# Optimization experiments

Measured on AMD Instinct MI355X. Metric: run time of the kernel, lower is better.

## Reference

```python
import jax, jax.numpy as jnp
import numpy as np

B, T, H, A, E, V = 32, 128, 1024, 1024, 512, 512  # A==H required by the module's cat/Linear shapes


def setup_inputs() -> dict:
    key = jax.random.key(0)
    ks = jax.random.split(key, 13)
    s = 0.02
    return {
        "encoder_outputs": jax.random.normal(ks[0], (B, A, E), jnp.float32),
        "hidden": jax.random.normal(ks[1], (1, B, H), jnp.float32),
        "target_seq": jax.random.normal(ks[2], (B, T, H), jnp.float32),
        "W_att": jax.random.normal(ks[3], (H + A, A), jnp.float32) * s,
        "b_att": jax.random.normal(ks[4], (A,), jnp.float32) * s,
        "W_comb": jax.random.normal(ks[5], (H + E, H), jnp.float32) * s,
        "b_comb": jax.random.normal(ks[6], (H,), jnp.float32) * s,
        "W_ih": jax.random.normal(ks[7], (3 * H, H), jnp.float32) * s,
        "b_ih": jax.random.normal(ks[8], (3 * H,), jnp.float32) * s,
        "W_hh": jax.random.normal(ks[9], (3 * H, H), jnp.float32) * s,
        "b_hh": jax.random.normal(ks[10], (3 * H,), jnp.float32) * s,
        "W_out": jax.random.normal(ks[11], (H, V), jnp.float32) * s,
        "b_out": jax.random.normal(ks[12], (V,), jnp.float32) * s,
    }


def reference(encoder_outputs, hidden, target_seq, W_att, b_att, W_comb, b_comb,
              W_ih, b_ih, W_hh, b_hh, W_out, b_out):
    # Teacher forcing: decoder input at step t is zeros (t=0) then target_seq[:, t-1]
    dec_in = jnp.concatenate([jnp.zeros_like(target_seq[:, :1]), target_seq[:, :-1]], axis=1)  # [B,T,H]
    dec_ts = jnp.swapaxes(dec_in, 0, 1)  # [T,B,H]

    def step(h, dec):  # h: [B,H], dec: [B,H]
        # attention over encoder positions (softmax width A == encoder seq len)
        attn = jax.nn.softmax(jnp.concatenate([dec, h], axis=1) @ W_att + b_att, axis=1)  # [B,A]
        ctx = jnp.einsum('bl,ble->be', attn, encoder_outputs)  # [B,E]
        g = jax.nn.relu(jnp.concatenate([dec, ctx], axis=1) @ W_comb + b_comb)  # [B,H]
        # GRU cell (torch gate order r, z, n)
        gi = g @ W_ih.T + b_ih
        gh = h @ W_hh.T + b_hh
        ir, iz, i_n = jnp.split(gi, 3, axis=1)
        hr, hz, h_n = jnp.split(gh, 3, axis=1)
        r = jax.nn.sigmoid(ir + hr)
        z = jax.nn.sigmoid(iz + hz)
        n = jnp.tanh(i_n + r * h_n)
        h_new = (1.0 - z) * n + z * h
        out_tok = h_new @ W_out + b_out  # [B,V]
        return h_new, out_tok

    h_last, outs = jax.lax.scan(step, hidden[0], dec_ts)  # outs: [T,B,V]
    output_seq = jnp.swapaxes(outs, 0, 1)  # [B,T,V]
    return output_seq, h_last[None]
```

## Files before the change

kernel.cpp:

```cpp
#include <hip/hip_runtime.h>

typedef unsigned short u16;
typedef unsigned int u32;
typedef unsigned long long u64;
typedef short v8s __attribute__((ext_vector_type(8)));
typedef float v4f __attribute__((ext_vector_type(4)));
typedef int v4i __attribute__((ext_vector_type(4)));

#define MFMA16(a, b, c) __builtin_amdgcn_mfma_f32_16x16x32_bf16((a), (b), (c), 0, 0, 0)

#define B_ 32
#define T_ 128
#define H_ 1024
#define A_ 1024
#define E_ 512
#define V_ 512
#define NBLK 256
#define NTH 512
#define NSLOT 32
#define ENC_LDS_BYTES 131072
#define SCRATCH_BYTES 28672
#define DSMEM_BYTES (ENC_LDS_BYTES + SCRATCH_BYTES)

__device__ __forceinline__ float b2f(u16 u) {
  union { u32 u; float f; } c; c.u = ((u32)u) << 16; return c.f;
}
__device__ __forceinline__ u16 f2b(float f) {
  union { float f; u32 u; } c; c.f = f;
  u32 x = c.u;
  x += 0x7fffu + ((x >> 16) & 1u);
  return (u16)(x >> 16);
}

__device__ __forceinline__ void ato_st(u32* p, u32 v) {
  __hip_atomic_store(p, v, __ATOMIC_RELAXED, __HIP_MEMORY_SCOPE_AGENT);
}
__device__ __forceinline__ void ato_stf(float* p, float v) {
  union { float f; u32 u; } c; c.f = v; ato_st((u32*)p, c.u);
}
__device__ __forceinline__ void ato_addf(float* p, float v) {
  __hip_atomic_fetch_add(p, v, __ATOMIC_RELAXED, __HIP_MEMORY_SCOPE_AGENT);
}

__device__ __forceinline__ v4i ld16_sc1(const void* p) {
  v4i r;
  asm volatile("global_load_dwordx4 %0, %1, off sc1" : "=v"(r) : "v"(p));
  return r;
}
__device__ __forceinline__ float ld4_sc1(const void* p) {
  float r;
  asm volatile("global_load_dword %0, %1, off sc1" : "=v"(r) : "v"(p));
  return r;
}
__device__ __forceinline__ void wait_vm0() {
  asm volatile("s_waitcnt vmcnt(0)" ::: "memory");
  __builtin_amdgcn_sched_barrier(0);
}
__device__ __forceinline__ v8s as8(v4i x) { union { v4i a; v8s b; } u; u.a = x; return u.b; }
__device__ __forceinline__ void cvt8(v4i qa, v4i qb, v8s& hi, v8s& lo) {
  union { v4i q; float f[4]; } a, b;
  a.q = qa; b.q = qb;
  float v[8] = {a.f[0], a.f[1], a.f[2], a.f[3], b.f[0], b.f[1], b.f[2], b.f[3]};
  u16 hh[8], ll[8];
  #pragma unroll
  for (int i = 0; i < 8; ++i) {
    float x = fmaxf(v[i], 0.f);
    u16 hv = f2b(x);
    hh[i] = hv; ll[i] = f2b(x - b2f(hv));
  }
  hi = *(v8s*)hh; lo = *(v8s*)ll;
}

__device__ __forceinline__ void grid_bar(u32* arr, u32 ep) {
  asm volatile("s_waitcnt vmcnt(0)" ::: "memory");
  __syncthreads();
  if (threadIdx.x == 0)
    __hip_atomic_store(arr + blockIdx.x * NSLOT, ep, __ATOMIC_RELAXED, __HIP_MEMORY_SCOPE_AGENT);
  if (threadIdx.x < NBLK) {
    while (__hip_atomic_load(arr + threadIdx.x * NSLOT, __ATOMIC_RELAXED, __HIP_MEMORY_SCOPE_AGENT) < ep)
      __builtin_amdgcn_s_sleep(1);
  }
  __syncthreads();
  asm volatile("" ::: "memory");
}

__device__ __forceinline__ void gemm_nk(const u16* ah, const u16* al, size_t mstr,
                                        const u16* bp, int nk, v4f& c0, v4f& c1) {
  #pragma unroll 2
  for (int i = 0; i < nk; ++i) {
    v8s b   = *(const v8s*)(bp);
    v8s a0h = *(const v8s*)(ah);
    v8s a1h = *(const v8s*)(ah + mstr);
    v8s a0l = *(const v8s*)(al);
    v8s a1l = *(const v8s*)(al + mstr);
    c0 = MFMA16(a0h, b, c0);
    c1 = MFMA16(a1h, b, c1);
    c0 = MFMA16(a0l, b, c0);
    c1 = MFMA16(a1l, b, c1);
    ah += 32; al += 32; bp += 32;
  }
}

__device__ __forceinline__ void red_store2(float* part, int wv, int lane, v4f c0, v4f c1) {
  float* p = part + (wv * 64 + lane) * 8;
  #pragma unroll
  for (int r = 0; r < 4; ++r) { p[r] = c0[r]; p[4 + r] = c1[r]; }
}
__device__ __forceinline__ float red_sum2(const float* part, int o) {
  int m = o >> 4, n = o & 15;
  int lane = (((m & 15) >> 2) << 4) + n;
  int idx = ((m >> 4) << 2) + (m & 3);
  float s = 0.f;
  #pragma unroll
  for (int w = 0; w < 8; ++w) s += part[(w * 64 + lane) * 8 + idx];
  return s;
}

__global__ void __launch_bounds__(NTH, 1)
dec_persist(const u16* __restrict__ tgt_hi, const u16* __restrict__ tgt_lo,
            const u16* __restrict__ WattT, const u16* __restrict__ Whh_b,
            const u16* __restrict__ Wih_b, const u16* __restrict__ WcombT,
            const u16* __restrict__ Wc_ctx,
            const float* __restrict__ enc_f,
            const float* __restrict__ batt, const float* __restrict__ bcomb,
            const float* __restrict__ bih, const float* __restrict__ bhh,
            float* h, float* logit, float* gh, float* g_acc, float* logit_dec,
            u16* hbf_hi, u16* hbf_lo, u16* hseqb, u32* bar)
{
  const int tid = threadIdx.x;
  const int bid = blockIdx.x;
  const int lane = tid & 63;
  const int wv = tid >> 6;
  const int ln = lane & 15;
  const int kq8 = (lane >> 4) * 8;

  extern __shared__ __align__(16) unsigned char dsm[];
  u16* lds_enc = (u16*)dsm;
  float* scratch = (float*)(dsm + ENC_LDS_BYTES);

  {
    int b = bid >> 3, e0 = (bid & 7) * 64;
    const float* src = enc_f + (size_t)b * A_ * E_ + e0 + (tid & 7) * 8;
    int seg = (tid & 7) * 8;
    for (int i = 0; i < 16; ++i) {
      int row = i * 64 + (tid >> 3);
      const float* sp = src + (size_t)row * E_;
      float4 a = *(const float4*)sp;
      float4 bq = *(const float4*)(sp + 4);
      u16 tmp[8] = {f2b(a.x), f2b(a.y), f2b(a.z), f2b(a.w),
                    f2b(bq.x), f2b(bq.y), f2b(bq.z), f2b(bq.w)};
      *(v8s*)(lds_enc + row * 64 + seg) = *(v8s*)tmp;
    }
  }

  u32 ep = 0;

  for (int t = 0; t < T_; ++t) {
    {
      float* part = scratch;
      size_t a0 = (size_t)ln * H_ + wv * 128 + kq8;
      v4i ah0[4], ah1[4], al0[4], al1[4];
      #pragma unroll
      for (int i = 0; i < 4; ++i) {
        ah0[i] = ld16_sc1(hbf_hi + a0 + i * 32);
        ah1[i] = ld16_sc1(hbf_hi + a0 + 16 * H_ + i * 32);
        al0[i] = ld16_sc1(hbf_lo + a0 + i * 32);
        al1[i] = ld16_sc1(hbf_lo + a0 + 16 * H_ + i * 32);
      }
      float ldec = 0.f;
      const u16* bp;
      int n0;
      if (bid < 64) {
        int gi = bid * 512 + tid;
        ato_stf(&g_acc[((t + 1) & 1) * (B_ * H_) + gi], bcomb[gi & (H_ - 1)]);
        n0 = bid * 16;
        ldec = ld4_sc1(&logit_dec[(t & 1) * (B_ * A_) + (tid >> 4) * A_ + n0 + (tid & 15)]);
        bp = WattT + (size_t)(n0 + ln) * 2048 + 1024 + wv * 128 + kq8;
      } else {
        n0 = (bid - 64) * 16;
        bp = Whh_b + (size_t)(n0 + ln) * H_ + wv * 128 + kq8;
      }
      v8s wb[4];
      #pragma unroll
      for (int i = 0; i < 4; ++i) wb[i] = *(const v8s*)(bp + i * 32);
      v4f c0 = {0.f, 0.f, 0.f, 0.f}, c1 = {0.f, 0.f, 0.f, 0.f};
      wait_vm0();
      #pragma unroll
      for (int i = 0; i < 4; ++i) {
        c0 = MFMA16(as8(ah0[i]), wb[i], c0);
        c1 = MFMA16(as8(ah1[i]), wb[i], c1);
        c0 = MFMA16(as8(al0[i]), wb[i], c0);
        c1 = MFMA16(as8(al1[i]), wb[i], c1);
      }
      red_store2(part, wv, lane, c0, c1);
      __syncthreads();
      {
        float s = red_sum2(part, tid);
        int m = tid >> 4, n = tid & 15;
        if (bid < 64) {
          ato_stf(&logit[m * A_ + n0 + n], s + ldec + batt[n0 + n]);
        } else {
          ato_stf(&gh[(size_t)(n0 + n) * 32 + m], s + bhh[n0 + n]);
        }
      }
    }
    grid_bar(bar, ++ep);

    {
      float* p    = scratch;
      float* part = scratch + 1024;
      float* red  = scratch + 5120;
      float* sctx = scratch + 5136;
      int b = bid >> 3, es = bid & 7;
      float v1 = ld4_sc1(&logit[b * A_ + tid]);
      float v2 = ld4_sc1(&logit[b * A_ + 512 + tid]);
      wait_vm0();
      float mx = fmaxf(v1, v2);
      #pragma unroll
      for (int off = 32; off; off >>= 1) mx = fmaxf(mx, __shfl_xor(mx, off));
      if (lane == 0) red[wv] = mx;
      __syncthreads();
      float mfull = red[0];
      #pragma unroll
      for (int q = 1; q < 8; ++q) mfull = fmaxf(mfull, red[q]);
      float e1 = __expf(v1 - mfull), e2 = __expf(v2 - mfull);
      p[tid] = e1; p[512 + tid] = e2;
      float sm = e1 + e2;
      #pragma unroll
      for (int off = 32; off; off >>= 1) sm += __shfl_xor(sm, off);
      if (lane == 0) red[8 + wv] = sm;
      __syncthreads();
      float ssum = red[8];
      #pragma unroll
      for (int q = 1; q < 8; ++q) ssum += red[8 + q];
      float inv = 1.f / ssum;

      int le = lane & 7, lr = lane >> 3;
      float acc[8] = {0.f, 0.f, 0.f, 0.f, 0.f, 0.f, 0.f, 0.f};
      #pragma unroll 4
      for (int i = 0; i < 16; ++i) {
        int l = i * 64 + wv * 8 + lr;
        v8s w = *(const v8s*)(lds_enc + l * 64 + le * 8);
        float pv = p[l];
        #pragma unroll
        for (int r = 0; r < 8; ++r) acc[r] += pv * b2f((u16)w[r]);
      }
      float* pp = part + ((wv * 8 + lr) * 8 + le) * 8;
      #pragma unroll
      for (int r = 0; r < 8; ++r) pp[r] = acc[r];
      __syncthreads();
      if (tid < 64) {
        int eo = tid >> 3, r = tid & 7;
        float s = 0.f;
        #pragma unroll
        for (int q = 0; q < 64; ++q) s += part[q * 64 + eo * 8 + r];
        sctx[tid] = s * inv;
      }
      __syncthreads();
      {
        const u16* wrow = Wc_ctx + (size_t)(es * 64) * H_ + tid * 2;
        float a0 = 0.f, a1 = 0.f;
        #pragma unroll 4
        for (int e = 0; e < 64; ++e) {
          u32 w = *(const u32*)(wrow + (size_t)e * H_);
          float pv = sctx[e];
          a0 += pv * b2f((u16)w);
          a1 += pv * b2f((u16)(w >> 16));
        }
        float* gp = g_acc + (t & 1) * (B_ * H_) + b * H_ + tid * 2;
        ato_addf(gp, a0);
        ato_addf(gp + 1, a1);
      }
    }
    grid_bar(bar, ++ep);

    {
      if (bid < 64) {
        float* part = scratch;
        float* hx   = scratch + 6144;
        int j0 = bid * 16;
        const float* gbase = g_acc + (t & 1) * (B_ * H_);
        int koff0 = wv * 128 + kq8;
        v4i gr0[8], gr1[8];
        #pragma unroll
        for (int i = 0; i < 4; ++i) {
          const float* p0 = gbase + (size_t)ln * H_ + koff0 + i * 32;
          const float* p1 = gbase + (size_t)(ln + 16) * H_ + koff0 + i * 32;
          gr0[2 * i]     = ld16_sc1(p0);
          gr0[2 * i + 1] = ld16_sc1(p0 + 4);
          gr1[2 * i]     = ld16_sc1(p1);
          gr1[2 * i + 1] = ld16_sc1(p1 + 4);
        }
        const u16* bp0 = Wih_b + (size_t)(j0 + ln) * H_ + koff0;
        const u16* bp1 = bp0 + (size_t)H_ * H_;
        const u16* bp2 = bp0 + (size_t)2 * H_ * H_;
        v8s wb0[4], wb1[4], wb2[4];
        #pragma unroll
        for (int i = 0; i < 4; ++i) {
          wb0[i] = *(const v8s*)(bp0 + i * 32);
          wb1[i] = *(const v8s*)(bp1 + i * 32);
          wb2[i] = *(const v8s*)(bp2 + i * 32);
        }
        v4f c00 = {0.f,0.f,0.f,0.f}, c01 = c00, c02 = c00, c10 = c00, c11 = c00, c12 = c00;
        wait_vm0();
        #pragma unroll
        for (int i = 0; i < 4; ++i) {
          v8s a0h, a0l, a1h, a1l;
          cvt8(gr0[2 * i], gr0[2 * i + 1], a0h, a0l);
          cvt8(gr1[2 * i], gr1[2 * i + 1], a1h, a1l);
          c00 = MFMA16(a0h, wb0[i], c00); c00 = MFMA16(a0l, wb0[i], c00);
          c01 = MFMA16(a0h, wb1[i], c01); c01 = MFMA16(a0l, wb1[i], c01);
          c02 = MFMA16(a0h, wb2[i], c02); c02 = MFMA16(a0l, wb2[i], c02);
          c10 = MFMA16(a1h, wb0[i], c10); c10 = MFMA16(a1l, wb0[i], c10);
          c11 = MFMA16(a1h, wb1[i], c11); c11 = MFMA16(a1l, wb1[i], c11);
          c12 = MFMA16(a1h, wb2[i], c12); c12 = MFMA16(a1l, wb2[i], c12);
        }
        float hr0 = 0.f, hz0 = 0.f, hn0 = 0.f, hr1 = 0.f, hz1 = 0.f, hn1 = 0.f;
        float ho0 = 0.f, ho1 = 0.f;
        int obl = tid >> 4, jj = tid & 15, j = j0 + jj;
        if (tid < 256) {
          hr0 = ld4_sc1(&gh[(size_t)j * 32 + obl]);
          hz0 = ld4_sc1(&gh[(size_t)(H_ + j) * 32 + obl]);
          hn0 = ld4_sc1(&gh[(size_t)(2 * H_ + j) * 32 + obl]);
          hr1 = ld4_sc1(&gh[(size_t)j * 32 + 16 + obl]);
          hz1 = ld4_sc1(&gh[(size_t)(H_ + j) * 32 + 16 + obl]);
          hn1 = ld4_sc1(&gh[(size_t)(2 * H_ + j) * 32 + 16 + obl]);
          ho0 = h[obl * H_ + j];
          ho1 = h[(obl + 16) * H_ + j];
        }
        float bi_r = 0.f, bi_z = 0.f, bi_n = 0.f;
        if (tid < 256) {
          bi_r = bih[j]; bi_z = bih[H_ + j]; bi_n = bih[2 * H_ + j];
        }
        #pragma unroll
        for (int pass = 0; pass < 2; ++pass) {
          float* pp = part + (wv * 64 + lane) * 12;
          if (pass == 0) {
            #pragma unroll
            for (int r = 0; r < 4; ++r) { pp[r] = c00[r]; pp[4 + r] = c01[r]; pp[8 + r] = c02[r]; }
          } else {
            #pragma unroll
            for (int r = 0; r < 4; ++r) { pp[r] = c10[r]; pp[4 + r] = c11[r]; pp[8 + r] = c12[r]; }
          }
          __syncthreads();
          if (tid < 256) {
            if (pass == 0) wait_vm0();
            int ob = pass * 16 + obl;
            int lanei = ((obl >> 2) << 4) + jj;
            int rg = obl & 3;
            float ir = 0.f, iz = 0.f, in_ = 0.f;
            #pragma unroll
            for (int w = 0; w < 8; ++w) {
              const float* q = part + (w * 64 + lanei) * 12;
              ir += q[rg]; iz += q[4 + rg]; in_ += q[8 + rg];
            }
            ir += bi_r; iz += bi_z; in_ += bi_n;
            float hr = pass ? hr1 : hr0;
            float hz = pass ? hz1 : hz0;
            float hn = pass ? hn1 : hn0;
            float ho = pass ? ho1 : ho0;
            float r = 1.f / (1.f + __expf(-(ir + hr)));
            float z = 1.f / (1.f + __expf(-(iz + hz)));
            float n = tanhf(in_ + r * hn);
            float hnew = (1.f - z) * n + z * ho;
            h[ob * H_ + j] = hnew;
            hx[ob * 16 + jj] = hnew;
          }
          __syncthreads();
        }
        if (tid < 256) {
          int ob2 = tid >> 3, j2 = (tid & 7) * 2;
          float v0 = hx[ob2 * 16 + j2], v1 = hx[ob2 * 16 + j2 + 1];
          u16 h0 = f2b(v0), h1 = f2b(v1);
          u16 l0 = f2b(v0 - b2f(h0)), l1 = f2b(v1 - b2f(h1));
          int idx = ob2 * H_ + j0 + j2;
          u32 hp = (u32)h0 | ((u32)h1 << 16);
          ato_st((u32*)(hbf_hi + idx), hp);
          ato_st((u32*)(hbf_lo + idx), (u32)l0 | ((u32)l1 << 16));
          *(u32*)(hseqb + ((size_t)t * 32 + ob2) * H_ + j0 + j2) = hp;
        }
      } else if (bid < 128) {
        if (t < T_ - 1) {
          float* part = scratch;
          int n0 = (bid - 64) * 16;
          v4f c0 = {0.f, 0.f, 0.f, 0.f}, c1 = {0.f, 0.f, 0.f, 0.f};
          size_t abase = ((size_t)ln * T_ + t) * H_ + wv * 128 + kq8;
          const u16* bp = WattT + (size_t)(n0 + ln) * 2048 + wv * 128 + kq8;
          gemm_nk(tgt_hi + abase, tgt_lo + abase, (size_t)16 * T_ * H_, bp, 4, c0, c1);
          red_store2(part, wv, lane, c0, c1);
          __syncthreads();
          int m = tid >> 4, n = tid & 15;
          ato_stf(&logit_dec[((t + 1) & 1) * (B_ * A_) + m * A_ + n0 + n], red_sum2(part, tid));
        }
      } else if (bid < 192) {
        if (t < T_ - 1) {
          float* part = scratch;
          int n0 = (bid - 128) * 16;
          v4f c0 = {0.f, 0.f, 0.f, 0.f}, c1 = {0.f, 0.f, 0.f, 0.f};
          size_t abase = ((size_t)ln * T_ + t) * H_ + wv * 128 + kq8;
          const u16* bp = WcombT + (size_t)(n0 + ln) * 1536 + wv * 128 + kq8;
          gemm_nk(tgt_hi + abase, tgt_lo + abase, (size_t)16 * T_ * H_, bp, 4, c0, c1);
          red_store2(part, wv, lane, c0, c1);
          __syncthreads();
          int m = tid >> 4, n = tid & 15;
          ato_addf(&g_acc[((t + 1) & 1) * (B_ * H_) + m * H_ + n0 + n], red_sum2(part, tid));
        }
      }
    }
    grid_bar(bar, ++ep);
  }
}

__global__ void __launch_bounds__(256, 2)
out_gemm(const u16* __restrict__ hseqb, const u16* __restrict__ WoutT,
         const float* __restrict__ bout, float* __restrict__ out)
{
  int tid = threadIdx.x, lane = tid & 63, wv = tid >> 6;
  int ln = lane & 15, kq8 = (lane >> 4) * 8;
  int m0 = (blockIdx.x >> 3) * 32;
  int n0 = (blockIdx.x & 7) * 64 + wv * 16;
  v4f c0 = {0.f, 0.f, 0.f, 0.f}, c1 = {0.f, 0.f, 0.f, 0.f};
  const u16* ap = hseqb + (size_t)(m0 + ln) * 1024 + kq8;
  const u16* bp = WoutT + (size_t)(n0 + ln) * 1024 + kq8;
  for (int i = 0; i < 32; ++i) {
    v8s b = *(const v8s*)bp;
    v8s a0 = *(const v8s*)ap;
    v8s a1 = *(const v8s*)(ap + 16 * 1024);
    c0 = MFMA16(a0, b, c0);
    c1 = MFMA16(a1, b, c1);
    ap += 32; bp += 32;
  }
  int v = n0 + ln;
  float bo = bout[v];
  int rbase = (lane >> 4) * 4;
  #pragma unroll
  for (int rg = 0; rg < 4; ++rg) {
    int m = m0 + rbase + rg;
    out[((size_t)(m & 31) * T_ + (m >> 5)) * V_ + v] = c0[rg] + bo;
    int m2 = m + 16;
    out[((size_t)(m2 & 31) * T_ + (m2 >> 5)) * V_ + v] = c1[rg] + bo;
  }
}

__global__ void __launch_bounds__(256)
hlast_copy(const float* __restrict__ h, float* __restrict__ out)
{
  int i = blockIdx.x * 256 + threadIdx.x;
  if (i < B_ * H_) out[(size_t)B_ * T_ * V_ + i] = h[i];
}

__global__ void __launch_bounds__(256)
k_cvt(const float* __restrict__ in, u16* __restrict__ out, int n)
{
  int stride = gridDim.x * 256;
  for (int i = blockIdx.x * 256 + threadIdx.x; i < n; i += stride) out[i] = f2b(in[i]);
}

__global__ void __launch_bounds__(256)
k_cvt_split(const float* __restrict__ in, u16* __restrict__ hi, u16* __restrict__ lo, int n)
{
  int stride = gridDim.x * 256;
  for (int i = blockIdx.x * 256 + threadIdx.x; i < n; i += stride) {
    float x = in[i];
    u16 a = f2b(x);
    hi[i] = a;
    lo[i] = f2b(x - b2f(a));
  }
}

__global__ void __launch_bounds__(256)
k_tr(const float* __restrict__ in, u16* __restrict__ out, int R, int C)
{
  __shared__ float tile[32][33];
  int tc = C >> 5;
  int r0 = (blockIdx.x / tc) << 5, c0 = (blockIdx.x % tc) << 5;
  int tx = threadIdx.x & 31, ty = threadIdx.x >> 5;
  #pragma unroll
  for (int q = 0; q < 4; ++q) {
    int r = ty + q * 8;
    tile[r][tx] = in[(size_t)(r0 + r) * C + c0 + tx];
  }
  __syncthreads();
  #pragma unroll
  for (int q = 0; q < 4; ++q) {
    int r = ty + q * 8;
    out[(size_t)(c0 + r) * R + r0 + tx] = f2b(tile[tx][r]);
  }
}

__global__ void __launch_bounds__(256)
k_init(const float* __restrict__ hidden, const float* __restrict__ bcomb,
       float* h, u16* hhi, u16* hlo, float* g_acc)
{
  int i = blockIdx.x * 256 + threadIdx.x;
  if (i < B_ * H_) {
    float x = hidden[i];
    h[i] = x;
    u16 a = f2b(x);
    hhi[i] = a;
    hlo[i] = f2b(x - b2f(a));
    g_acc[i] = bcomb[i & (H_ - 1)];
  }
}

extern "C" void kernel_launch(void* const* d_in, const int* in_sizes, int n_in,
                              void* d_out, int out_size, void* d_ws, size_t ws_size,
                              hipStream_t stream) {
  (void)in_sizes; (void)n_in; (void)out_size; (void)ws_size;
  const float* enc    = (const float*)d_in[0];
  const float* hidden = (const float*)d_in[1];
  const float* tgt    = (const float*)d_in[2];
  const float* Watt   = (const float*)d_in[3];
  const float* batt   = (const float*)d_in[4];
  const float* Wcomb  = (const float*)d_in[5];
  const float* bcomb  = (const float*)d_in[6];
  const float* Wih    = (const float*)d_in[7];
  const float* bih    = (const float*)d_in[8];
  const float* Whh    = (const float*)d_in[9];
  const float* bhh    = (const float*)d_in[10];
  const float* Wout   = (const float*)d_in[11];
  const float* bout   = (const float*)d_in[12];

  size_t off = 0;
  char* base = (char*)d_ws;
  auto alloc = [&](size_t bytes) -> void* {
    void* p = base + off;
    off += (bytes + 255) & ~(size_t)255;
    return p;
  };
  size_t bar_bytes = (size_t)(NBLK * NSLOT + NSLOT) * 4;
  u32*   bar    = (u32*)  alloc(bar_bytes);
  float* h      = (float*)alloc(B_ * H_ * 4);
  float* logit  = (float*)alloc(B_ * A_ * 4);
  float* gh     = (float*)alloc((size_t)3 * H_ * B_ * 4);
  float* g_acc  = (float*)alloc((size_t)2 * B_ * H_ * 4);
  float* logit_dec = (float*)alloc((size_t)2 * B_ * A_ * 4);
  u16*   hbf_hi = (u16*)  alloc(B_ * H_ * 2);
  u16*   hbf_lo = (u16*)  alloc(B_ * H_ * 2);
  u16*   hseqb  = (u16*)  alloc((size_t)T_ * B_ * H_ * 2);
  u16*   tgt_hi = (u16*)  alloc((size_t)B_ * T_ * H_ * 2);
  u16*   tgt_lo = (u16*)  alloc((size_t)B_ * T_ * H_ * 2);
  u16*   WattT  = (u16*)  alloc((size_t)2048 * 1024 * 2);
  u16*   Whh_b  = (u16*)  alloc((size_t)3 * H_ * H_ * 2);
  u16*   Wih_b  = (u16*)  alloc((size_t)3 * H_ * H_ * 2);
  u16*   WcombT = (u16*)  alloc((size_t)1024 * 1536 * 2);
  u16*   Wc_ctx = (u16*)  alloc((size_t)512 * 1024 * 2);
  u16*   WoutT  = (u16*)  alloc((size_t)512 * 1024 * 2);

  hipMemsetAsync(bar, 0, bar_bytes, stream);
  hipMemsetAsync(logit_dec, 0, (size_t)2 * B_ * A_ * 4, stream);

  k_cvt_split<<<2048, 256, 0, stream>>>(tgt, tgt_hi, tgt_lo, B_ * T_ * H_);
  k_cvt<<<2048, 256, 0, stream>>>(Whh, Whh_b, 3 * H_ * H_);
  k_cvt<<<2048, 256, 0, stream>>>(Wih, Wih_b, 3 * H_ * H_);
  k_cvt<<<2048, 256, 0, stream>>>(Wcomb + (size_t)1024 * H_, Wc_ctx, 512 * H_);
  k_tr<<<64 * 32, 256, 0, stream>>>(Watt, WattT, 2048, 1024);
  k_tr<<<48 * 32, 256, 0, stream>>>(Wcomb, WcombT, 1536, 1024);
  k_tr<<<32 * 16, 256, 0, stream>>>(Wout, WoutT, 1024, 512);
  k_init<<<128, 256, 0, stream>>>(hidden, bcomb, h, hbf_hi, hbf_lo, g_acc);

  hipFuncSetAttribute((const void*)dec_persist,
                      hipFuncAttributeMaxDynamicSharedMemorySize, DSMEM_BYTES);

  dec_persist<<<NBLK, NTH, DSMEM_BYTES, stream>>>(tgt_hi, tgt_lo, WattT, Whh_b, Wih_b,
                                                  WcombT, Wc_ctx, enc,
                                                  batt, bcomb, bih, bhh,
                                                  h, logit, gh, g_acc, logit_dec,
                                                  hbf_hi, hbf_lo, hseqb, bar);
  out_gemm<<<1024, 256, 0, stream>>>(hseqb, WoutT, bout, (float*)d_out);
  hlast_copy<<<128, 256, 0, stream>>>(h, (float*)d_out);
}
```

Baseline: 3.641 ms.

## Hoist teacher-forced input GEMMs out of persistent loop; add two-level grid barrier

The decoder-input projections through W_att and W_comb no longer run inside the persistent recurrent kernel. They are now computed for all timesteps by a separate batched GEMM kernel into full-sequence buffers, with the biases folded in, so each step only reads a precomputed value. The grid barrier becomes two-level: 8 aggregator blocks each watch 32 block flags, and every block then polls only 8 flags. The context-weight matrix is transposed so each thread reads it with vector loads. The cost is larger workspace buffers and two extra kernel launches, in exchange for less per-step work and less barrier polling.

```diff
diff --git a/kernel.cpp b/kernel.cpp
--- a/kernel.cpp
+++ b/kernel.cpp
@@ -18,6 +18,7 @@
 #define NBLK 256
 #define NTH 512
 #define NSLOT 32
+#define AGGB 248
 #define ENC_LDS_BYTES 131072
 #define SCRATCH_BYTES 28672
 #define DSMEM_BYTES (ENC_LDS_BYTES + SCRATCH_BYTES)
@@ -72,12 +73,23 @@
 }
 
 __device__ __forceinline__ void grid_bar(u32* arr, u32 ep) {
+  u32* lvl2 = arr + NBLK * NSLOT;
   asm volatile("s_waitcnt vmcnt(0)" ::: "memory");
   __syncthreads();
   if (threadIdx.x == 0)
     __hip_atomic_store(arr + blockIdx.x * NSLOT, ep, __ATOMIC_RELAXED, __HIP_MEMORY_SCOPE_AGENT);
-  if (threadIdx.x < NBLK) {
-    while (__hip_atomic_load(arr + threadIdx.x * NSLOT, __ATOMIC_RELAXED, __HIP_MEMORY_SCOPE_AGENT) < ep)
+  if (blockIdx.x >= AGGB) {
+    int g = blockIdx.x - AGGB;
+    if (threadIdx.x < 32) {
+      while (__hip_atomic_load(arr + (g * 32 + threadIdx.x) * NSLOT,
+                               __ATOMIC_RELAXED, __HIP_MEMORY_SCOPE_AGENT) < ep)
+        __builtin_amdgcn_s_sleep(1);
+    }
+    if (threadIdx.x == 0)
+      __hip_atomic_store(lvl2 + g, ep, __ATOMIC_RELAXED, __HIP_MEMORY_SCOPE_AGENT);
+  }
+  if (threadIdx.x < 8) {
+    while (__hip_atomic_load(lvl2 + threadIdx.x, __ATOMIC_RELAXED, __HIP_MEMORY_SCOPE_AGENT) < ep)
       __builtin_amdgcn_s_sleep(1);
   }
   __syncthreads();
@@ -117,14 +129,12 @@
 }
 
 __global__ void __launch_bounds__(NTH, 1)
-dec_persist(const u16* __restrict__ tgt_hi, const u16* __restrict__ tgt_lo,
-            const u16* __restrict__ WattT, const u16* __restrict__ Whh_b,
-            const u16* __restrict__ Wih_b, const u16* __restrict__ WcombT,
-            const u16* __restrict__ Wc_ctx,
+dec_persist(const u16* __restrict__ WattT, const u16* __restrict__ Whh_b,
+            const u16* __restrict__ Wih_b, const u16* __restrict__ Wc_ctxT,
             const float* __restrict__ enc_f,
-            const float* __restrict__ batt, const float* __restrict__ bcomb,
             const float* __restrict__ bih, const float* __restrict__ bhh,
-            float* h, float* logit, float* gh, float* g_acc, float* logit_dec,
+            const float* __restrict__ ldec_all,
+            float* h, float* logit, float* gh, float* g_all,
             u16* hbf_hi, u16* hbf_lo, u16* hseqb, u32* bar)
 {
   const int tid = threadIdx.x;
@@ -171,10 +181,8 @@
       const u16* bp;
       int n0;
       if (bid < 64) {
-        int gi = bid * 512 + tid;
-        ato_stf(&g_acc[((t + 1) & 1) * (B_ * H_) + gi], bcomb[gi & (H_ - 1)]);
         n0 = bid * 16;
-        ldec = ld4_sc1(&logit_dec[(t & 1) * (B_ * A_) + (tid >> 4) * A_ + n0 + (tid & 15)]);
+        ldec = ldec_all[(size_t)t * (B_ * A_) + (tid >> 4) * A_ + n0 + (tid & 15)];
         bp = WattT + (size_t)(n0 + ln) * 2048 + 1024 + wv * 128 + kq8;
       } else {
         n0 = (bid - 64) * 16;
@@ -198,7 +206,7 @@
         float s = red_sum2(part, tid);
         int m = tid >> 4, n = tid & 15;
         if (bid < 64) {
-          ato_stf(&logit[m * A_ + n0 + n], s + ldec + batt[n0 + n]);
+          ato_stf(&logit[m * A_ + n0 + n], s + ldec);
         } else {
           ato_stf(&gh[(size_t)(n0 + n) * 32 + m], s + bhh[n0 + n]);
         }
@@ -258,16 +266,21 @@
       }
       __syncthreads();
       {
-        const u16* wrow = Wc_ctx + (size_t)(es * 64) * H_ + tid * 2;
+        const u16* w0 = Wc_ctxT + (size_t)(2 * tid) * E_ + es * 64;
+        const u16* w1 = w0 + E_;
         float a0 = 0.f, a1 = 0.f;
-        #pragma unroll 4
-        for (int e = 0; e < 64; ++e) {
-          u32 w = *(const u32*)(wrow + (size_t)e * H_);
-          float pv = sctx[e];
-          a0 += pv * b2f((u16)w);
-          a1 += pv * b2f((u16)(w >> 16));
-        }
-        float* gp = g_acc + (t & 1) * (B_ * H_) + b * H_ + tid * 2;
+        #pragma unroll
+        for (int i = 0; i < 8; ++i) {
+          v8s q0 = *(const v8s*)(w0 + i * 8);
+          v8s q1 = *(const v8s*)(w1 + i * 8);
+          #pragma unroll
+          for (int r = 0; r < 8; ++r) {
+            float pv = sctx[i * 8 + r];
+            a0 += pv * b2f((u16)q0[r]);
+            a1 += pv * b2f((u16)q1[r]);
+          }
+        }
+        float* gp = g_all + (size_t)t * (B_ * H_) + b * H_ + 2 * tid;
         ato_addf(gp, a0);
         ato_addf(gp + 1, a1);
       }
@@ -279,7 +292,7 @@
         float* part = scratch;
         float* hx   = scratch + 6144;
         int j0 = bid * 16;
-        const float* gbase = g_acc + (t & 1) * (B_ * H_);
+        const float* gbase = g_all + (size_t)t * (B_ * H_);
         int koff0 = wv * 128 + kq8;
         v4i gr0[8], gr1[8];
         #pragma unroll
@@ -379,35 +392,41 @@
           ato_st((u32*)(hbf_lo + idx), (u32)l0 | ((u32)l1 << 16));
           *(u32*)(hseqb + ((size_t)t * 32 + ob2) * H_ + j0 + j2) = hp;
         }
-      } else if (bid < 128) {
-        if (t < T_ - 1) {
-          float* part = scratch;
-          int n0 = (bid - 64) * 16;
-          v4f c0 = {0.f, 0.f, 0.f, 0.f}, c1 = {0.f, 0.f, 0.f, 0.f};
-          size_t abase = ((size_t)ln * T_ + t) * H_ + wv * 128 + kq8;
-          const u16* bp = WattT + (size_t)(n0 + ln) * 2048 + wv * 128 + kq8;
-          gemm_nk(tgt_hi + abase, tgt_lo + abase, (size_t)16 * T_ * H_, bp, 4, c0, c1);
-          red_store2(part, wv, lane, c0, c1);
-          __syncthreads();
-          int m = tid >> 4, n = tid & 15;
-          ato_stf(&logit_dec[((t + 1) & 1) * (B_ * A_) + m * A_ + n0 + n], red_sum2(part, tid));
-        }
-      } else if (bid < 192) {
-        if (t < T_ - 1) {
-          float* part = scratch;
-          int n0 = (bid - 128) * 16;
-          v4f c0 = {0.f, 0.f, 0.f, 0.f}, c1 = {0.f, 0.f, 0.f, 0.f};
-          size_t abase = ((size_t)ln * T_ + t) * H_ + wv * 128 + kq8;
-          const u16* bp = WcombT + (size_t)(n0 + ln) * 1536 + wv * 128 + kq8;
-          gemm_nk(tgt_hi + abase, tgt_lo + abase, (size_t)16 * T_ * H_, bp, 4, c0, c1);
-          red_store2(part, wv, lane, c0, c1);
-          __syncthreads();
-          int m = tid >> 4, n = tid & 15;
-          ato_addf(&g_acc[((t + 1) & 1) * (B_ * H_) + m * H_ + n0 + n], red_sum2(part, tid));
-        }
       }
     }
     grid_bar(bar, ++ep);
+  }
+}
+
+__global__ void __launch_bounds__(256)
+dec_gemm(const u16* __restrict__ th, const u16* __restrict__ tl,
+         const u16* __restrict__ W, const unsigned long wstride,
+         const float* __restrict__ bias, float* __restrict__ out)
+{
+  int tid = threadIdx.x, lane = tid & 63, wv = tid >> 6;
+  int ln = lane & 15, kq8 = (lane >> 4) * 8;
+  int t = blockIdx.x >> 4, nt = blockIdx.x & 15;
+  float* op = out + (size_t)t * (32 * 1024);
+  if (t == 0) {
+    for (int i = tid; i < 32 * 64; i += 256) {
+      int b = i >> 6, n = nt * 64 + (i & 63);
+      op[(size_t)b * 1024 + n] = bias[n];
+    }
+    return;
+  }
+  int n0w = nt * 64 + wv * 16;
+  const u16* ah = th + ((size_t)ln * T_ + (t - 1)) * H_ + kq8;
+  const u16* al = tl + ((size_t)ln * T_ + (t - 1)) * H_ + kq8;
+  const u16* bp = W + (size_t)(n0w + ln) * wstride + kq8;
+  v4f c0 = {0.f, 0.f, 0.f, 0.f}, c1 = {0.f, 0.f, 0.f, 0.f};
+  gemm_nk(ah, al, (size_t)16 * T_ * H_, bp, 32, c0, c1);
+  int n = n0w + (lane & 15);
+  float bo = bias[n];
+  int rb = (lane >> 4) * 4;
+  #pragma unroll
+  for (int r = 0; r < 4; ++r) {
+    op[(size_t)(rb + r) * 1024 + n] = c0[r] + bo;
+    op[(size_t)(rb + r + 16) * 1024 + n] = c1[r] + bo;
   }
 }
 
@@ -489,8 +508,7 @@
 }
 
 __global__ void __launch_bounds__(256)
-k_init(const float* __restrict__ hidden, const float* __restrict__ bcomb,
-       float* h, u16* hhi, u16* hlo, float* g_acc)
+k_init(const float* __restrict__ hidden, float* h, u16* hhi, u16* hlo)
 {
   int i = blockIdx.x * 256 + threadIdx.x;
   if (i < B_ * H_) {
@@ -499,7 +517,6 @@
     u16 a = f2b(x);
     hhi[i] = a;
     hlo[i] = f2b(x - b2f(a));
-    g_acc[i] = bcomb[i & (H_ - 1)];
   }
 }
 
@@ -528,13 +545,13 @@
     off += (bytes + 255) & ~(size_t)255;
     return p;
   };
-  size_t bar_bytes = (size_t)(NBLK * NSLOT + NSLOT) * 4;
+  size_t bar_bytes = (size_t)(NBLK * NSLOT + 64) * 4;
   u32*   bar    = (u32*)  alloc(bar_bytes);
   float* h      = (float*)alloc(B_ * H_ * 4);
   float* logit  = (float*)alloc(B_ * A_ * 4);
   float* gh     = (float*)alloc((size_t)3 * H_ * B_ * 4);
-  float* g_acc  = (float*)alloc((size_t)2 * B_ * H_ * 4);
-  float* logit_dec = (float*)alloc((size_t)2 * B_ * A_ * 4);
+  float* ldec_all = (float*)alloc((size_t)T_ * B_ * A_ * 4);
+  float* g_all    = (float*)alloc((size_t)T_ * B_ * H_ * 4);
   u16*   hbf_hi = (u16*)  alloc(B_ * H_ * 2);
   u16*   hbf_lo = (u16*)  alloc(B_ * H_ * 2);
   u16*   hseqb  = (u16*)  alloc((size_t)T_ * B_ * H_ * 2);
@@ -544,28 +561,29 @@
   u16*   Whh_b  = (u16*)  alloc((size_t)3 * H_ * H_ * 2);
   u16*   Wih_b  = (u16*)  alloc((size_t)3 * H_ * H_ * 2);
   u16*   WcombT = (u16*)  alloc((size_t)1024 * 1536 * 2);
-  u16*   Wc_ctx = (u16*)  alloc((size_t)512 * 1024 * 2);
+  u16*   Wc_ctxT= (u16*)  alloc((size_t)1024 * 512 * 2);
   u16*   WoutT  = (u16*)  alloc((size_t)512 * 1024 * 2);
 
   hipMemsetAsync(bar, 0, bar_bytes, stream);
-  hipMemsetAsync(logit_dec, 0, (size_t)2 * B_ * A_ * 4, stream);
 
   k_cvt_split<<<2048, 256, 0, stream>>>(tgt, tgt_hi, tgt_lo, B_ * T_ * H_);
   k_cvt<<<2048, 256, 0, stream>>>(Whh, Whh_b, 3 * H_ * H_);
   k_cvt<<<2048, 256, 0, stream>>>(Wih, Wih_b, 3 * H_ * H_);
-  k_cvt<<<2048, 256, 0, stream>>>(Wcomb + (size_t)1024 * H_, Wc_ctx, 512 * H_);
   k_tr<<<64 * 32, 256, 0, stream>>>(Watt, WattT, 2048, 1024);
   k_tr<<<48 * 32, 256, 0, stream>>>(Wcomb, WcombT, 1536, 1024);
+  k_tr<<<16 * 32, 256, 0, stream>>>(Wcomb + (size_t)1024 * H_, Wc_ctxT, 512, 1024);
   k_tr<<<32 * 16, 256, 0, stream>>>(Wout, WoutT, 1024, 512);
-  k_init<<<128, 256, 0, stream>>>(hidden, bcomb, h, hbf_hi, hbf_lo, g_acc);
+  k_init<<<128, 256, 0, stream>>>(hidden, h, hbf_hi, hbf_lo);
+
+  dec_gemm<<<2048, 256, 0, stream>>>(tgt_hi, tgt_lo, WattT, 2048UL, batt, ldec_all);
+  dec_gemm<<<2048, 256, 0, stream>>>(tgt_hi, tgt_lo, WcombT, 1536UL, bcomb, g_all);
 
   hipFuncSetAttribute((const void*)dec_persist,
                       hipFuncAttributeMaxDynamicSharedMemorySize, DSMEM_BYTES);
 
-  dec_persist<<<NBLK, NTH, DSMEM_BYTES, stream>>>(tgt_hi, tgt_lo, WattT, Whh_b, Wih_b,
-                                                  WcombT, Wc_ctx, enc,
-                                                  batt, bcomb, bih, bhh,
-                                                  h, logit, gh, g_acc, logit_dec,
+  dec_persist<<<NBLK, NTH, DSMEM_BYTES, stream>>>(WattT, Whh_b, Wih_b, Wc_ctxT, enc,
+                                                  bih, bhh, ldec_all,
+                                                  h, logit, gh, g_all,
                                                   hbf_hi, hbf_lo, hseqb, bar);
   out_gemm<<<1024, 256, 0, stream>>>(hseqb, WoutT, bout, (float*)d_out);
   hlast_copy<<<128, 256, 0, stream>>>(h, (float*)d_out);
```

New measurement: 4.405 ms. +21.0%, slower.

## Replace full grid barriers with producer-subset semaphores and transpose ctx weights

Applied to the files above, without the earlier changes.

Each of the three full grid barriers per timestep becomes a semaphore: only the blocks that produce data post to it, and only the blocks that consume it wait. Stage 2 is only awaited by the first 64 blocks. The attention bias add moves into the precomputed logit_dec term so it leaves the critical path. The context-combine weights are stored transposed so each thread reads contiguous 16-byte vectors instead of strided u32 loads. The risk is that the narrower waits must still cover every data dependency, including buffer reuse across timesteps, and the spin now sleeps longer between polls.

```diff
diff --git a/kernel.cpp b/kernel.cpp
--- a/kernel.cpp
+++ b/kernel.cpp
@@ -71,14 +71,16 @@
   hi = *(v8s*)hh; lo = *(v8s*)ll;
 }
 
-__device__ __forceinline__ void grid_bar(u32* arr, u32 ep) {
+__device__ __forceinline__ void post_sem(u32* slots, int idx, u32 ep) {
   asm volatile("s_waitcnt vmcnt(0)" ::: "memory");
   __syncthreads();
   if (threadIdx.x == 0)
-    __hip_atomic_store(arr + blockIdx.x * NSLOT, ep, __ATOMIC_RELAXED, __HIP_MEMORY_SCOPE_AGENT);
-  if (threadIdx.x < NBLK) {
-    while (__hip_atomic_load(arr + threadIdx.x * NSLOT, __ATOMIC_RELAXED, __HIP_MEMORY_SCOPE_AGENT) < ep)
-      __builtin_amdgcn_s_sleep(1);
+    __hip_atomic_store(slots + idx * NSLOT, ep, __ATOMIC_RELAXED, __HIP_MEMORY_SCOPE_AGENT);
+}
+__device__ __forceinline__ void wait_sem(const u32* slots, int n, u32 ep) {
+  if (threadIdx.x < (unsigned)n) {
+    while (__hip_atomic_load(slots + threadIdx.x * NSLOT, __ATOMIC_RELAXED, __HIP_MEMORY_SCOPE_AGENT) < ep)
+      __builtin_amdgcn_s_sleep(8);
   }
   __syncthreads();
   asm volatile("" ::: "memory");
@@ -120,12 +122,12 @@
 dec_persist(const u16* __restrict__ tgt_hi, const u16* __restrict__ tgt_lo,
             const u16* __restrict__ WattT, const u16* __restrict__ Whh_b,
             const u16* __restrict__ Wih_b, const u16* __restrict__ WcombT,
-            const u16* __restrict__ Wc_ctx,
+            const u16* __restrict__ Wc_ctxT,
             const float* __restrict__ enc_f,
             const float* __restrict__ batt, const float* __restrict__ bcomb,
             const float* __restrict__ bih, const float* __restrict__ bhh,
             float* h, float* logit, float* gh, float* g_acc, float* logit_dec,
-            u16* hbf_hi, u16* hbf_lo, u16* hseqb, u32* bar)
+            u16* hbf_hi, u16* hbf_lo, u16* hseqb, u32* sems)
 {
   const int tid = threadIdx.x;
   const int bid = blockIdx.x;
@@ -133,6 +135,10 @@
   const int wv = tid >> 6;
   const int ln = lane & 15;
   const int kq8 = (lane >> 4) * 8;
+
+  u32* S1 = sems;
+  u32* S2 = sems + 64 * NSLOT;
+  u32* S3 = sems + (64 + 256) * NSLOT;
 
   extern __shared__ __align__(16) unsigned char dsm[];
   u16* lds_enc = (u16*)dsm;
@@ -153,9 +159,8 @@
     }
   }
 
-  u32 ep = 0;
-
   for (int t = 0; t < T_; ++t) {
+    u32 ep = (u32)(t + 1);
     {
       float* part = scratch;
       size_t a0 = (size_t)ln * H_ + wv * 128 + kq8;
@@ -198,13 +203,14 @@
         float s = red_sum2(part, tid);
         int m = tid >> 4, n = tid & 15;
         if (bid < 64) {
-          ato_stf(&logit[m * A_ + n0 + n], s + ldec + batt[n0 + n]);
+          ato_stf(&logit[m * A_ + n0 + n], s + ldec);
         } else {
           ato_stf(&gh[(size_t)(n0 + n) * 32 + m], s + bhh[n0 + n]);
         }
       }
     }
-    grid_bar(bar, ++ep);
+    if (bid < 64) post_sem(S1, bid, ep);
+    wait_sem(S1, 64, ep);
 
     {
       float* p    = scratch;
@@ -258,21 +264,27 @@
       }
       __syncthreads();
       {
-        const u16* wrow = Wc_ctx + (size_t)(es * 64) * H_ + tid * 2;
+        const u16* w0 = Wc_ctxT + (size_t)(2 * tid) * E_ + es * 64;
+        const u16* w1 = w0 + E_;
         float a0 = 0.f, a1 = 0.f;
-        #pragma unroll 4
-        for (int e = 0; e < 64; ++e) {
-          u32 w = *(const u32*)(wrow + (size_t)e * H_);
-          float pv = sctx[e];
-          a0 += pv * b2f((u16)w);
-          a1 += pv * b2f((u16)(w >> 16));
-        }
-        float* gp = g_acc + (t & 1) * (B_ * H_) + b * H_ + tid * 2;
+        #pragma unroll
+        for (int i = 0; i < 8; ++i) {
+          v8s q0 = *(const v8s*)(w0 + i * 8);
+          v8s q1 = *(const v8s*)(w1 + i * 8);
+          #pragma unroll
+          for (int r = 0; r < 8; ++r) {
+            float pv = sctx[i * 8 + r];
+            a0 += pv * b2f((u16)q0[r]);
+            a1 += pv * b2f((u16)q1[r]);
+          }
+        }
+        float* gp = g_acc + (t & 1) * (B_ * H_) + b * H_ + 2 * tid;
         ato_addf(gp, a0);
         ato_addf(gp + 1, a1);
       }
     }
-    grid_bar(bar, ++ep);
+    post_sem(S2, bid, ep);
+    if (bid < 64) wait_sem(S2, NBLK, ep);
 
     {
       if (bid < 64) {
@@ -390,7 +402,8 @@
           red_store2(part, wv, lane, c0, c1);
           __syncthreads();
           int m = tid >> 4, n = tid & 15;
-          ato_stf(&logit_dec[((t + 1) & 1) * (B_ * A_) + m * A_ + n0 + n], red_sum2(part, tid));
+          ato_stf(&logit_dec[((t + 1) & 1) * (B_ * A_) + m * A_ + n0 + n],
+                  red_sum2(part, tid) + batt[n0 + n]);
         }
       } else if (bid < 192) {
         if (t < T_ - 1) {
@@ -407,7 +420,8 @@
         }
       }
     }
-    grid_bar(bar, ++ep);
+    if (bid < 192) post_sem(S3, bid, ep);
+    wait_sem(S3, 192, ep);
   }
 }
 
@@ -528,8 +542,8 @@
     off += (bytes + 255) & ~(size_t)255;
     return p;
   };
-  size_t bar_bytes = (size_t)(NBLK * NSLOT + NSLOT) * 4;
-  u32*   bar    = (u32*)  alloc(bar_bytes);
+  size_t sem_bytes = (size_t)(64 + 256 + 192) * NSLOT * 4;
+  u32*   sems   = (u32*)  alloc(sem_bytes);
   float* h      = (float*)alloc(B_ * H_ * 4);
   float* logit  = (float*)alloc(B_ * A_ * 4);
   float* gh     = (float*)alloc((size_t)3 * H_ * B_ * 4);
@@ -544,18 +558,18 @@
   u16*   Whh_b  = (u16*)  alloc((size_t)3 * H_ * H_ * 2);
   u16*   Wih_b  = (u16*)  alloc((size_t)3 * H_ * H_ * 2);
   u16*   WcombT = (u16*)  alloc((size_t)1024 * 1536 * 2);
-  u16*   Wc_ctx = (u16*)  alloc((size_t)512 * 1024 * 2);
+  u16*   Wc_ctxT= (u16*)  alloc((size_t)1024 * 512 * 2);
   u16*   WoutT  = (u16*)  alloc((size_t)512 * 1024 * 2);
 
-  hipMemsetAsync(bar, 0, bar_bytes, stream);
+  hipMemsetAsync(sems, 0, sem_bytes, stream);
   hipMemsetAsync(logit_dec, 0, (size_t)2 * B_ * A_ * 4, stream);
 
   k_cvt_split<<<2048, 256, 0, stream>>>(tgt, tgt_hi, tgt_lo, B_ * T_ * H_);
   k_cvt<<<2048, 256, 0, stream>>>(Whh, Whh_b, 3 * H_ * H_);
   k_cvt<<<2048, 256, 0, stream>>>(Wih, Wih_b, 3 * H_ * H_);
-  k_cvt<<<2048, 256, 0, stream>>>(Wcomb + (size_t)1024 * H_, Wc_ctx, 512 * H_);
   k_tr<<<64 * 32, 256, 0, stream>>>(Watt, WattT, 2048, 1024);
   k_tr<<<48 * 32, 256, 0, stream>>>(Wcomb, WcombT, 1536, 1024);
+  k_tr<<<16 * 32, 256, 0, stream>>>(Wcomb + (size_t)1024 * H_, Wc_ctxT, 512, 1024);
   k_tr<<<32 * 16, 256, 0, stream>>>(Wout, WoutT, 1024, 512);
   k_init<<<128, 256, 0, stream>>>(hidden, bcomb, h, hbf_hi, hbf_lo, g_acc);
 
@@ -563,10 +577,10 @@
                       hipFuncAttributeMaxDynamicSharedMemorySize, DSMEM_BYTES);
 
   dec_persist<<<NBLK, NTH, DSMEM_BYTES, stream>>>(tgt_hi, tgt_lo, WattT, Whh_b, Wih_b,
-                                                  WcombT, Wc_ctx, enc,
+                                                  WcombT, Wc_ctxT, enc,
                                                   batt, bcomb, bih, bhh,
                                                   h, logit, gh, g_acc, logit_dec,
-                                                  hbf_hi, hbf_lo, hseqb, bar);
+                                                  hbf_hi, hbf_lo, hseqb, sems);
   out_gemm<<<1024, 256, 0, stream>>>(hseqb, WoutT, bout, (float*)d_out);
   hlast_copy<<<128, 256, 0, stream>>>(h, (float*)d_out);
 }
```

After: 3.936 ms. 8.1% more time.
